# Performance work log

Hardware: AMD Instinct MI355X
Metric: run time of the kernel (lower is better)

## Reference

```python
import jax, jax.numpy as jnp
import numpy as np

B, L, D = 2, 2048, 2048
H, G, HS = 32, 8, 64  # n_heads, n_query_groups, head_size
NEG = -1e30


def setup_inputs() -> dict:
    key = jax.random.key(0)
    ks = jax.random.split(key, 7)
    s = 1.0 / np.sqrt(D)
    return {
        "x": jax.random.normal(ks[0], (B, L, D), jnp.float32),
        "cos": jax.random.uniform(ks[1], (L, HS), jnp.float32),
        "sin": jax.random.uniform(ks[2], (L, HS), jnp.float32),
        "Wq": jax.random.normal(ks[3], (D, D), jnp.float32) * s,
        "Wk": jax.random.normal(ks[4], (G * HS, D), jnp.float32) * s,
        "Wv": jax.random.normal(ks[5], (G * HS, D), jnp.float32) * s,
        "Wo": jax.random.normal(ks[6], (D, D), jnp.float32) * s,
    }


def _apply_rope(t, cos, sin):
    # t: (B, h, L, HS); cos/sin: (L, HS) broadcast over (B, h)
    x1, x2 = t[..., : HS // 2], t[..., HS // 2 :]
    rotated = jnp.concatenate((-x2, x1), axis=-1)
    return (t * cos + rotated * sin).astype(t.dtype)


def reference(x, cos, sin, Wq, Wk, Wv, Wo):
    # projections (torch Linear: y = x @ W.T)
    q = jnp.einsum("bld,ed->ble", x, Wq).reshape(B, L, H, HS).transpose(0, 2, 1, 3)
    k = jnp.einsum("bld,ed->ble", x, Wk).reshape(B, L, G, HS).transpose(0, 2, 1, 3)
    v = jnp.einsum("bld,ed->ble", x, Wv).reshape(B, L, G, HS).transpose(0, 2, 1, 3)
    q = _apply_rope(q, cos, sin)
    k = _apply_rope(k, cos, sin)
    # GQA expand: each group repeated H//G consecutive times (matches expand+reshape)
    k = jnp.repeat(k, H // G, axis=1)
    v = jnp.repeat(v, H // G, axis=1)
    scale = 1.0 / np.sqrt(HS)
    scores = jnp.einsum("bhqd,bhkd->bhqk", q, k) * scale
    causal = jnp.tril(jnp.ones((L, L), bool))
    scores = jnp.where(causal, scores, NEG)
    attn = jax.nn.softmax(scores, axis=-1)
    o = jnp.einsum("bhqk,bhkd->bhqd", attn, v)  # (B,H,L,HS)
    o = o.transpose(0, 2, 1, 3).reshape(B, L, D)
    return jnp.einsum("bld,ed->ble", o, Wo)
```

## Files before the change

### kernel.cpp

```cpp
#include <hip/hip_runtime.h>

typedef __bf16 bf16;
typedef __bf16 bf16x4 __attribute__((ext_vector_type(4)));
typedef __bf16 bf16x8 __attribute__((ext_vector_type(8)));
typedef float  f32x4  __attribute__((ext_vector_type(4)));
typedef float  f32x16 __attribute__((ext_vector_type(16)));

#define GLDS16(gsrc, ldst)                                                    \
  __builtin_amdgcn_global_load_lds(                                          \
      (const __attribute__((address_space(1))) void*)(gsrc),                 \
      (__attribute__((address_space(3))) void*)(ldst), 16, 0, 0)

#define MFMA16(a, b, c) __builtin_amdgcn_mfma_f32_16x16x32_bf16((a), (b), (c), 0, 0, 0)
#define MFMA32(a, b, c) __builtin_amdgcn_mfma_f32_32x32x16_bf16((a), (b), (c), 0, 0, 0)
#define PLSWAP(a, b) asm volatile("v_permlane32_swap_b32 %0, %1" : "+v"(a), "+v"(b))

__device__ inline unsigned pk2(float a, float b) {
  union { bf16 h[2]; unsigned u; } t;
  t.h[0] = (bf16)a; t.h[1] = (bf16)b;
  return t.u;
}
__device__ inline float ex2(float x) { return __builtin_amdgcn_exp2f(x); }

__global__ __launch_bounds__(256) void cvt5_kernel(const float* __restrict__ x,
                                                   const float* __restrict__ wq,
                                                   const float* __restrict__ wk,
                                                   const float* __restrict__ wv,
                                                   const float* __restrict__ wo,
                                                   bf16* __restrict__ xb,
                                                   bf16* __restrict__ wqkv,
                                                   bf16* __restrict__ wob) {
  int i = blockIdx.x * 256 + threadIdx.x;
  const float* src; bf16* dst; int off;
  if (i < 2097152)      { src = x;  dst = xb;             off = i; }
  else if (i < 3145728) { src = wq; dst = wqkv;           off = i - 2097152; }
  else if (i < 3407872) { src = wk; dst = wqkv + 4194304; off = i - 3145728; }
  else if (i < 3670016) { src = wv; dst = wqkv + 5242880; off = i - 3407872; }
  else                  { src = wo; dst = wob;            off = i - 3670016; }
  f32x4 f = *(const f32x4*)(src + (size_t)off * 4);
  bf16x4 o4;
#pragma unroll
  for (int j = 0; j < 4; ++j) o4[j] = (bf16)f[j];
  *(bf16x4*)(dst + (size_t)off * 4) = o4;
}

__global__ __launch_bounds__(256) void vtr_kernel(const bf16* __restrict__ v,
                                                  bf16* __restrict__ vt) {
  constexpr int L = 2048, QS = 3072;
  const int kv0 = blockIdx.x * 64;
  const int bg = blockIdx.y;
  const int tid = threadIdx.x;
  __shared__ bf16 t[64 * 64];

#pragma unroll
  for (int i = 0; i < 2; ++i) {
    int c = tid + 256 * i;
    int kv = c >> 3, e = c & 7;
    bf16x8 row = *(const bf16x8*)(v + (size_t)((bg >> 3) * L + kv0 + kv) * QS +
                                  (bg & 7) * 64 + e * 8);
#pragma unroll
    for (int j = 0; j < 8; ++j)
      t[(8 * e + j) * 64 + (kv ^ (8 * (e ^ j)))] = row[j];
  }
  __syncthreads();

  const int d = tid >> 2, c4 = tid & 3;
  bf16* orow = vt + ((size_t)bg * 64 + d) * L + kv0;
#pragma unroll
  for (int dl = 0; dl < 2; ++dl) {
    int sc = 2 * c4 + dl;
    bf16x8 ch = *(const bf16x8*)&t[d * 64 + 8 * (sc ^ (d >> 3))];
    *(bf16x8*)(orow + 8 * sc) = ch;
  }
}

template <typename OutT, bool ROPE>
__global__ __launch_bounds__(256) void gemm_bt32(const bf16* __restrict__ A,
                                                 const bf16* __restrict__ Bm,
                                                 OutT* __restrict__ C,
                                                 int M, int N, int K,
                                                 const float* __restrict__ cosb,
                                                 const float* __restrict__ sinb) {
  __shared__ bf16 a_lds[128 * 32];
  __shared__ bf16 b_lds[128 * 32];
  const int tid = threadIdx.x;
  const int w = tid >> 6, lane = tid & 63;
  const int lr = lane & 15, lg = lane >> 4;
  const int wr = w >> 1, wc = w & 1;
  const int nbx = N >> 7;
  const int nwg = (M >> 7) * nbx;
  const int bid = blockIdx.x;
  const int sid = (bid & 7) * (nwg >> 3) + (bid >> 3);
  const int m0 = (sid / nbx) << 7, n0 = (sid % nbx) << 7;

  f32x4 acc[4][4];
#pragma unroll
  for (int i = 0; i < 4; ++i)
#pragma unroll
    for (int j = 0; j < 4; ++j) acc[i][j] = f32x4{0.f, 0.f, 0.f, 0.f};

  const int srow = tid >> 2, skc = (tid & 3) * 8;
  const bf16* ap0 = A  + (size_t)(m0 + srow) * K + skc;
  const bf16* ap1 = A  + (size_t)(m0 + srow + 64) * K + skc;
  const bf16* bp0 = Bm + (size_t)(n0 + srow) * K + skc;
  const bf16* bp1 = Bm + (size_t)(n0 + srow + 64) * K + skc;
  bf16* const lA0 = &a_lds[w * 512];
  bf16* const lA1 = &a_lds[w * 512 + 2048];
  bf16* const lB0 = &b_lds[w * 512];
  bf16* const lB1 = &b_lds[w * 512 + 2048];

  for (int kt = 0; kt < K; kt += 32) {
    GLDS16(ap0, lA0);
    GLDS16(ap1, lA1);
    GLDS16(bp0, lB0);
    GLDS16(bp1, lB1);
    ap0 += 32; ap1 += 32; bp0 += 32; bp1 += 32;
    __syncthreads();
    bf16x8 af[4], bfr[4];
#pragma unroll
    for (int t = 0; t < 4; ++t) {
      af[t]  = *(const bf16x8*)&a_lds[(wr * 64 + t * 16 + lr) * 32 + lg * 8];
      bfr[t] = *(const bf16x8*)&b_lds[(wc * 64 + t * 16 + lr) * 32 + lg * 8];
    }
#pragma unroll
    for (int mt = 0; mt < 4; ++mt)
#pragma unroll
      for (int nt = 0; nt < 4; ++nt)
        acc[mt][nt] = MFMA16(af[mt], bfr[nt], acc[mt][nt]);
    __syncthreads();
  }

  const int hb = (n0 + wc * 64) >> 6;
  const bool dorope = ROPE && (hb < 40);
  const float rsc = (ROPE && hb < 32) ? 0.18033688011112042f : 1.0f;

#pragma unroll
  for (int mt = 0; mt < 4; ++mt)
#pragma unroll
    for (int r = 0; r < 4; ++r) {
      int mm = m0 + wr * 64 + mt * 16 + 4 * lg + r;
      float ov[4];
      if (dorope) {
        int l = mm & 2047;
        const float* cp = cosb + l * 64 + lr;
        const float* sp = sinb + l * 64 + lr;
        float a0 = acc[mt][0][r], a1 = acc[mt][1][r];
        float a2 = acc[mt][2][r], a3 = acc[mt][3][r];
        ov[0] = (a0 * cp[0]  - a2 * sp[0])  * rsc;
        ov[1] = (a1 * cp[16] - a3 * sp[16]) * rsc;
        ov[2] = (a2 * cp[32] + a0 * sp[32]) * rsc;
        ov[3] = (a3 * cp[48] + a1 * sp[48]) * rsc;
      } else {
#pragma unroll
        for (int nt = 0; nt < 4; ++nt) ov[nt] = acc[mt][nt][r];
      }
#pragma unroll
      for (int nt = 0; nt < 4; ++nt) {
        int nn = n0 + wc * 64 + nt * 16 + lr;
        C[(size_t)mm * N + nn] = (OutT)ov[nt];
      }
    }
}

template <typename OutT>
__global__ __launch_bounds__(256) void gemm_bt64(const bf16* __restrict__ A,
                                                 const bf16* __restrict__ Bm,
                                                 OutT* __restrict__ C,
                                                 int M, int N, int K) {
  __shared__ bf16 a_lds[128 * 64];
  __shared__ bf16 b_lds[128 * 64];
  const int tid = threadIdx.x;
  const int w = tid >> 6, lane = tid & 63;
  const int lr = lane & 15, lg = lane >> 4;
  const int wr = w >> 1, wc = w & 1;
  const int nbx = N >> 7;
  const int nwg = (M >> 7) * nbx;
  const int bid = blockIdx.x;
  const int sid = (bid & 7) * (nwg >> 3) + (bid >> 3);
  const int m0 = (sid / nbx) << 7, n0 = (sid % nbx) << 7;

  f32x4 acc[4][4];
#pragma unroll
  for (int i = 0; i < 4; ++i)
#pragma unroll
    for (int j = 0; j < 4; ++j) acc[i][j] = f32x4{0.f, 0.f, 0.f, 0.f};

  const bf16* ap[4];
  const bf16* bp[4];
#pragma unroll
  for (int i = 0; i < 4; ++i) {
    int ci = tid + 256 * i;
    int row = ci >> 3, c = ci & 7;
    int cs = c ^ (row & 7);
    ap[i] = A  + (size_t)(m0 + row) * K + cs * 8;
    bp[i] = Bm + (size_t)(n0 + row) * K + cs * 8;
  }

  for (int kt = 0; kt < K; kt += 64) {
#pragma unroll
    for (int i = 0; i < 4; ++i) {
      GLDS16(ap[i], &a_lds[w * 512 + i * 2048]);
      GLDS16(bp[i], &b_lds[w * 512 + i * 2048]);
      ap[i] += 64; bp[i] += 64;
    }
    __syncthreads();
    bf16x8 af[4][2], bfr[4][2];
#pragma unroll
    for (int t = 0; t < 4; ++t) {
      int ra = wr * 64 + t * 16 + lr;
      int rb = wc * 64 + t * 16 + lr;
#pragma unroll
      for (int kc = 0; kc < 2; ++kc) {
        af[t][kc]  = *(const bf16x8*)&a_lds[ra * 64 + (((4 * kc + lg) ^ (ra & 7)) * 8)];
        bfr[t][kc] = *(const bf16x8*)&b_lds[rb * 64 + (((4 * kc + lg) ^ (rb & 7)) * 8)];
      }
    }
#pragma unroll
    for (int mt = 0; mt < 4; ++mt)
#pragma unroll
      for (int nt = 0; nt < 4; ++nt)
#pragma unroll
        for (int kc = 0; kc < 2; ++kc)
          acc[mt][nt] = MFMA16(af[mt][kc], bfr[nt][kc], acc[mt][nt]);
    __syncthreads();
  }

#pragma unroll
  for (int mt = 0; mt < 4; ++mt)
#pragma unroll
    for (int r = 0; r < 4; ++r) {
      int mm = m0 + wr * 64 + mt * 16 + 4 * lg + r;
#pragma unroll
      for (int nt = 0; nt < 4; ++nt) {
        int nn = n0 + wc * 64 + nt * 16 + lr;
        C[(size_t)mm * N + nn] = (OutT)acc[mt][nt][r];
      }
    }
}

__global__ __launch_bounds__(256, 4) void attn_kernel(const bf16* __restrict__ q,
                                                      const bf16* __restrict__ k,
                                                      const bf16* __restrict__ vtg,
                                                      bf16* __restrict__ o,
                                                      bf16* __restrict__ opart,
                                                      float* __restrict__ mpart,
                                                      float* __restrict__ lpart,
                                                      int split_n, int umax) {
  constexpr int L = 2048;
  constexpr int QS = 3072;
  constexpr int OS = 2048;
  const int id = blockIdx.x;
  int bh, u, ts, te, pidx;
  bool split;
  if (id < split_n) {
    bh = id & 63;
    int t = id >> 6;
    u = 15 - (t >> 1);
    int s = t & 1;
    ts = s * (u + 1);
    te = ts + (u + 1);
    pidx = (bh * 9 + (u - 7)) * 2 + s;
    split = true;
  } else {
    int e = id - split_n;
    bh = e & 63;
    u = umax - (e >> 6);
    ts = 0;
    te = 2 * u + 2;
    pidx = 0;
    split = false;
  }
  const int q0 = u * 128;
  const int b = bh >> 5, h = bh & 31, g = h >> 2;
  const int tid = threadIdx.x;
  const int w = tid >> 6, lane = tid & 63;
  const int lc = lane & 31;
  const int H  = lane >> 5;
  const int off4 = 4 * H;
  const int qw = q0 + w * 32;
  const int qg = qw + lc;

  __shared__ bf16 k_lds[2][64 * 64];
  __shared__ bf16 vt_lds[2][64 * 64];

  bf16x8 qf[4];
  {
    const bf16* qrow = q + (size_t)(b * L + qg) * QS + h * 64 + 8 * H;
#pragma unroll
    for (int s = 0; s < 4; ++s) qf[s] = *(const bf16x8*)(qrow + 16 * s);
  }

  f32x16 acc0, acc1;
#pragma unroll
  for (int r = 0; r < 16; ++r) { acc0[r] = 0.f; acc1[r] = 0.f; }
  float m_run = -1e30f, l_run = 0.f;

  const bf16* vbase = vtg + (size_t)(b * 8 + g) * 64 * L;

  const int kvr = tid >> 3, c8 = tid & 7;
  const bf16* kp0 = k + (size_t)(b * L + ts * 64 + kvr) * QS + g * 64 + ((c8 ^ (kvr & 7)) * 8);
  const bf16* kp1 = kp0 + (size_t)32 * QS;
  const bf16* vp0 = vbase + (size_t)kvr * L + ts * 64 + c8 * 8;
  const bf16* vp1 = vp0 + (size_t)32 * L;

  auto stageK = [&](int buf) {
    GLDS16(kp0, &k_lds[buf][w * 512]);
    GLDS16(kp1, &k_lds[buf][w * 512 + 2048]);
    kp0 += (size_t)64 * QS; kp1 += (size_t)64 * QS;
  };
  auto stageV = [&](int buf) {
    GLDS16(vp0, &vt_lds[buf][w * 512]);
    GLDS16(vp1, &vt_lds[buf][w * 512 + 2048]);
    vp0 += 64; vp1 += 64;
  };

  stageK(0);
  stageV(0);
  __syncthreads();

  for (int it = ts; it < te; ++it) {
    const int cur = (it - ts) & 1;
    const int kv0 = it * 64;
    const bool notlast = (it + 1 < te);
    if (notlast) {
      stageK(cur ^ 1);
      stageV(cur ^ 1);
    }

    if (kv0 <= qw + 31) {
      f32x16 p0, p1;
#pragma unroll
      for (int r = 0; r < 16; ++r) { p0[r] = 0.f; p1[r] = 0.f; }
      __builtin_amdgcn_s_setprio(1);
#pragma unroll
      for (int s = 0; s < 4; ++s) {
        int ch = ((2 * s + H) ^ (lc & 7)) * 8;
        bf16x8 kf0 = *(const bf16x8*)&k_lds[cur][lc * 64 + ch];
        bf16x8 kf1 = *(const bf16x8*)&k_lds[cur][(32 + lc) * 64 + ch];
        p0 = MFMA32(kf0, qf[s], p0);
        p1 = MFMA32(kf1, qf[s], p1);
      }
      __builtin_amdgcn_s_setprio(0);

      if (kv0 + 63 > qw) {
#pragma unroll
        for (int r = 0; r < 16; ++r) {
          int kvl = kv0 + (r & 3) + 8 * (r >> 2) + off4;
          if (kvl > qg)      p0[r] = -1e30f;
          if (kvl + 32 > qg) p1[r] = -1e30f;
        }
      }

      float mt = -1e30f;
#pragma unroll
      for (int r = 0; r < 16; ++r) mt = fmaxf(mt, fmaxf(p0[r], p1[r]));
      mt = fmaxf(mt, __shfl_xor(mt, 32));
      const int defer = __all(mt <= m_run + 11.0f);
      float alpha = 1.f;
      if (!defer) {
        float mn = fmaxf(m_run, mt);
        alpha = ex2(m_run - mn);
        m_run = mn;
      }
      float ls = 0.f;
#pragma unroll
      for (int r = 0; r < 16; ++r) {
        p0[r] = ex2(p0[r] - m_run);
        p1[r] = ex2(p1[r] - m_run);
        ls += p0[r] + p1[r];
      }
      ls += __shfl_xor(ls, 32);
      l_run = l_run * alpha + ls;
      if (!defer) {
#pragma unroll
        for (int r = 0; r < 16; ++r) {
          float aq = __shfl(alpha, ((r & 3) + 8 * (r >> 2)) + off4);
          acc0[r] *= aq;
          acc1[r] *= aq;
        }
      }

      unsigned A[16];
#pragma unroll
      for (int i = 0; i < 8; ++i) {
        A[i]     = pk2(p0[2 * i], p0[2 * i + 1]);
        A[8 + i] = pk2(p1[2 * i], p1[2 * i + 1]);
      }
#pragma unroll
      for (int base = 0; base < 16; base += 4) {
        PLSWAP(A[base],     A[base + 2]);
        PLSWAP(A[base + 1], A[base + 3]);
      }

      __builtin_amdgcn_s_setprio(1);
#pragma unroll
      for (int sp = 0; sp < 4; ++sp) {
        union { unsigned u[4]; bf16x8 v8; } pa;
#pragma unroll
        for (int jx = 0; jx < 4; ++jx) pa.u[jx] = A[4 * sp + jx];
        int ch = ((2 * sp + H) ^ (lc & 7)) * 8;
        bf16x8 vf0 = *(const bf16x8*)&vt_lds[cur][lc * 64 + ch];
        bf16x8 vf1 = *(const bf16x8*)&vt_lds[cur][(32 + lc) * 64 + ch];
        acc0 = MFMA32(pa.v8, vf0, acc0);
        acc1 = MFMA32(pa.v8, vf1, acc1);
      }
      __builtin_amdgcn_s_setprio(0);
    }

    __syncthreads();
  }

  if (split) {
    bf16* op = opart + (size_t)pidx * (128 * 64);
#pragma unroll
    for (int r = 0; r < 16; ++r) {
      int qrow = w * 32 + (r & 3) + 8 * (r >> 2) + off4;
      op[qrow * 64 + lc]      = (bf16)acc0[r];
      op[qrow * 64 + 32 + lc] = (bf16)acc1[r];
    }
    if (H == 0) {
      mpart[(size_t)pidx * 128 + w * 32 + lc] = m_run;
      lpart[(size_t)pidx * 128 + w * 32 + lc] = l_run;
    }
  } else {
#pragma unroll
    for (int r = 0; r < 16; ++r) {
      int qrow = (r & 3) + 8 * (r >> 2) + off4;
      float lq = __shfl(l_run, qrow);
      float inv = 1.f / lq;
      size_t orow = (size_t)(b * L + qw + qrow) * OS + h * 64;
      o[orow + lc]      = (bf16)(acc0[r] * inv);
      o[orow + 32 + lc] = (bf16)(acc1[r] * inv);
    }
  }
}

__global__ __launch_bounds__(256) void comb_kernel(const bf16* __restrict__ opart,
                                                   const float* __restrict__ mpart,
                                                   const float* __restrict__ lpart,
                                                   bf16* __restrict__ o) {
  constexpr int L = 2048, OS = 2048;
  const int blk = blockIdx.x;
  const int bh = blk / 9, uu = blk % 9, u = uu + 7;
  const int b = bh >> 5, h = bh & 31;
  const int q0 = u * 128;
  const int t = threadIdx.x;
  const int row = t >> 1, dh = (t & 1) * 32;

  const size_t s0 = (size_t)blk * 2, s1 = s0 + 1;
  float m0 = mpart[s0 * 128 + row], m1 = mpart[s1 * 128 + row];
  float l0 = lpart[s0 * 128 + row], l1 = lpart[s1 * 128 + row];
  float m = fmaxf(m0, m1);
  float w0 = ex2(m0 - m), w1 = ex2(m1 - m);
  float inv = 1.f / (l0 * w0 + l1 * w1);

  const bf16* O0 = opart + s0 * (128 * 64) + row * 64 + dh;
  const bf16* O1 = opart + s1 * (128 * 64) + row * 64 + dh;
  bf16* orow = o + (size_t)(b * L + q0 + row) * OS + h * 64 + dh;
#pragma unroll
  for (int j = 0; j < 4; ++j) {
    bf16x8 a = *(const bf16x8*)(O0 + 8 * j);
    bf16x8 c = *(const bf16x8*)(O1 + 8 * j);
    bf16x8 r;
#pragma unroll
    for (int e = 0; e < 8; ++e)
      r[e] = (bf16)(((float)a[e] * w0 + (float)c[e] * w1) * inv);
    *(bf16x8*)(orow + 8 * j) = r;
  }
}

extern "C" void kernel_launch(void* const* d_in, const int* in_sizes, int n_in,
                              void* d_out, int out_size, void* d_ws, size_t ws_size,
                              hipStream_t stream) {
  (void)in_sizes; (void)n_in; (void)out_size;
  const float* x    = (const float*)d_in[0];
  const float* cosb = (const float*)d_in[1];
  const float* sinb = (const float*)d_in[2];
  const float* Wq   = (const float*)d_in[3];
  const float* Wk   = (const float*)d_in[4];
  const float* Wv   = (const float*)d_in[5];
  const float* Wo   = (const float*)d_in[6];

  constexpr int B = 2, L = 2048, D = 2048, H = 32, G = 8;
  constexpr int M = B * L;
  constexpr int DKV = G * 64;
  constexpr int NQKV = D + 2 * DKV;

  char* p = (char*)d_ws;
  bf16*  xb   = (bf16*)p;  p += (size_t)M * D * 2;
  bf16*  wqkv = (bf16*)p;  p += (size_t)NQKV * D * 2;
  bf16*  wob  = (bf16*)p;  p += (size_t)D * D * 2;
  bf16*  qkv  = (bf16*)p;  p += (size_t)M * NQKV * 2;
  bf16*  vtg  = (bf16*)p;  p += (size_t)B * G * 64 * L * 2;
  bf16*  opart = (bf16*)p; p += (size_t)1152 * 128 * 64 * 2;
  float* mpart = (float*)p; p += (size_t)1152 * 128 * 4;
  float* lpart = (float*)p; p += (size_t)1152 * 128 * 4;
  bf16*  ob   = xb;

  const bool do_split = ws_size >= (size_t)(p - (char*)d_ws);

  cvt5_kernel<<<dim3(18432), 256, 0, stream>>>(x, Wq, Wk, Wv, Wo, xb, wqkv, wob);

  gemm_bt32<bf16, true><<<dim3((NQKV / 128) * (M / 128)), 256, 0, stream>>>(
      xb, wqkv, qkv, M, NQKV, D, cosb, sinb);

  vtr_kernel<<<dim3(L / 64, B * G), 256, 0, stream>>>(qkv + D + DKV, vtg);

  if (do_split) {
    attn_kernel<<<dim3(1600), 256, 0, stream>>>(qkv, qkv + D, vtg, ob,
                                                opart, mpart, lpart, 1152, 6);
    comb_kernel<<<dim3(576), 256, 0, stream>>>(opart, mpart, lpart, ob);
  } else {
    attn_kernel<<<dim3(1024), 256, 0, stream>>>(qkv, qkv + D, vtg, ob,
                                                opart, mpart, lpart, 0, 15);
  }

  gemm_bt64<float><<<dim3((D / 128) * (M / 128)), 256, 0, stream>>>(
      ob, wob, (float*)d_out, M, D, D);
}
```

Before: 213.6 us.

## Split long causal attention rows into 2-4 KV chunks for better balance

Adds a finer split-KV schedule: query tiles u>=12 split into 4 KV chunks, 8-11 into 3, 4-7 into 2, with short tiles unsplit, giving 2560 attention blocks. The combine kernel is generalized to merge a variable number of partials per row. This aims to reduce tail imbalance from the causal triangle, at the cost of more partial-output traffic and workspace, falling back to the old schedule if workspace is too small.

```diff
diff --git a/kernel.cpp b/kernel.cpp
--- a/kernel.cpp
+++ b/kernel.cpp
@@ -245,30 +245,52 @@
                                                       bf16* __restrict__ opart,
                                                       float* __restrict__ mpart,
                                                       float* __restrict__ lpart,
-                                                      int split_n, int umax) {
+                                                      int mode) {
   constexpr int L = 2048;
   constexpr int QS = 3072;
   constexpr int OS = 2048;
   const int id = blockIdx.x;
-  int bh, u, ts, te, pidx;
+  int bh, u, t0, t1, pidx;
   bool split;
-  if (id < split_n) {
+  if (mode == 2) {
+    if (id < 2304) {
+      bh = id & 63;
+      int j = id >> 6, s, ns;
+      if (j < 16)      { u = 15 - (j >> 2); s = j & 3; ns = 4; }
+      else if (j < 28) { int jj = j - 16; u = 11 - jj / 3; s = jj % 3; ns = 3; }
+      else             { int jj = j - 28; u = 7 - (jj >> 1); s = jj & 1; ns = 2; }
+      int T = 2 * u + 2;
+      t0 = s * T / ns;
+      t1 = (s + 1) * T / ns;
+      int basep = (u >= 12) ? 4 * u - 28 : (u >= 8) ? 3 * u - 16 : 2 * u - 8;
+      pidx = bh * 36 + basep + s;
+      split = true;
+    } else {
+      int e = id - 2304;
+      bh = e & 63;
+      u = 3 - (e >> 6);
+      t0 = 0; t1 = 2 * u + 2; pidx = 0; split = false;
+    }
+  } else if (mode == 1) {
+    if (id < 1152) {
+      bh = id & 63;
+      int t = id >> 6;
+      u = 15 - (t >> 1);
+      int s = t & 1;
+      t0 = s * (u + 1);
+      t1 = t0 + (u + 1);
+      pidx = (bh * 9 + (u - 7)) * 2 + s;
+      split = true;
+    } else {
+      int e = id - 1152;
+      bh = e & 63;
+      u = 6 - (e >> 6);
+      t0 = 0; t1 = 2 * u + 2; pidx = 0; split = false;
+    }
+  } else {
     bh = id & 63;
-    int t = id >> 6;
-    u = 15 - (t >> 1);
-    int s = t & 1;
-    ts = s * (u + 1);
-    te = ts + (u + 1);
-    pidx = (bh * 9 + (u - 7)) * 2 + s;
-    split = true;
-  } else {
-    int e = id - split_n;
-    bh = e & 63;
-    u = umax - (e >> 6);
-    ts = 0;
-    te = 2 * u + 2;
-    pidx = 0;
-    split = false;
+    u = 15 - (id >> 6);
+    t0 = 0; t1 = 2 * u + 2; pidx = 0; split = false;
   }
   const int q0 = u * 128;
   const int b = bh >> 5, h = bh & 31, g = h >> 2;
@@ -298,9 +320,9 @@
   const bf16* vbase = vtg + (size_t)(b * 8 + g) * 64 * L;
 
   const int kvr = tid >> 3, c8 = tid & 7;
-  const bf16* kp0 = k + (size_t)(b * L + ts * 64 + kvr) * QS + g * 64 + ((c8 ^ (kvr & 7)) * 8);
+  const bf16* kp0 = k + (size_t)(b * L + t0 * 64 + kvr) * QS + g * 64 + ((c8 ^ (kvr & 7)) * 8);
   const bf16* kp1 = kp0 + (size_t)32 * QS;
-  const bf16* vp0 = vbase + (size_t)kvr * L + ts * 64 + c8 * 8;
+  const bf16* vp0 = vbase + (size_t)kvr * L + t0 * 64 + c8 * 8;
   const bf16* vp1 = vp0 + (size_t)32 * L;
 
   auto stageK = [&](int buf) {
@@ -318,10 +340,10 @@
   stageV(0);
   __syncthreads();
 
-  for (int it = ts; it < te; ++it) {
-    const int cur = (it - ts) & 1;
+  for (int it = t0; it < t1; ++it) {
+    const int cur = (it - t0) & 1;
     const int kv0 = it * 64;
-    const bool notlast = (it + 1 < te);
+    const bool notlast = (it + 1 < t1);
     if (notlast) {
       stageK(cur ^ 1);
       stageV(cur ^ 1);
@@ -438,33 +460,52 @@
 __global__ __launch_bounds__(256) void comb_kernel(const bf16* __restrict__ opart,
                                                    const float* __restrict__ mpart,
                                                    const float* __restrict__ lpart,
-                                                   bf16* __restrict__ o) {
+                                                   bf16* __restrict__ o, int mode) {
   constexpr int L = 2048, OS = 2048;
   const int blk = blockIdx.x;
-  const int bh = blk / 9, uu = blk % 9, u = uu + 7;
+  int u, bh, ns;
+  size_t slot0;
+  if (mode == 2) {
+    u = 4 + blk % 12;
+    bh = blk / 12;
+    ns = (u >= 12) ? 4 : (u >= 8) ? 3 : 2;
+    int basep = (u >= 12) ? 4 * u - 28 : (u >= 8) ? 3 * u - 16 : 2 * u - 8;
+    slot0 = (size_t)bh * 36 + basep;
+  } else {
+    u = 7 + blk % 9;
+    bh = blk / 9;
+    ns = 2;
+    slot0 = ((size_t)bh * 9 + (u - 7)) * 2;
+  }
   const int b = bh >> 5, h = bh & 31;
   const int q0 = u * 128;
   const int t = threadIdx.x;
   const int row = t >> 1, dh = (t & 1) * 32;
 
-  const size_t s0 = (size_t)blk * 2, s1 = s0 + 1;
-  float m0 = mpart[s0 * 128 + row], m1 = mpart[s1 * 128 + row];
-  float l0 = lpart[s0 * 128 + row], l1 = lpart[s1 * 128 + row];
-  float m = fmaxf(m0, m1);
-  float w0 = ex2(m0 - m), w1 = ex2(m1 - m);
-  float inv = 1.f / (l0 * w0 + l1 * w1);
-
-  const bf16* O0 = opart + s0 * (128 * 64) + row * 64 + dh;
-  const bf16* O1 = opart + s1 * (128 * 64) + row * 64 + dh;
+  float m = -1e30f;
+  for (int s = 0; s < ns; ++s) m = fmaxf(m, mpart[(slot0 + s) * 128 + row]);
+  float wgt[4];
+  float l = 0.f;
+  for (int s = 0; s < ns; ++s) {
+    wgt[s] = ex2(mpart[(slot0 + s) * 128 + row] - m);
+    l += lpart[(slot0 + s) * 128 + row] * wgt[s];
+  }
+  float inv = 1.f / l;
+
   bf16* orow = o + (size_t)(b * L + q0 + row) * OS + h * 64 + dh;
 #pragma unroll
   for (int j = 0; j < 4; ++j) {
-    bf16x8 a = *(const bf16x8*)(O0 + 8 * j);
-    bf16x8 c = *(const bf16x8*)(O1 + 8 * j);
+    float a8[8];
+#pragma unroll
+    for (int e = 0; e < 8; ++e) a8[e] = 0.f;
+    for (int s = 0; s < ns; ++s) {
+      bf16x8 a = *(const bf16x8*)(opart + (slot0 + s) * 8192 + row * 64 + dh + 8 * j);
+#pragma unroll
+      for (int e = 0; e < 8; ++e) a8[e] += (float)a[e] * wgt[s];
+    }
     bf16x8 r;
 #pragma unroll
-    for (int e = 0; e < 8; ++e)
-      r[e] = (bf16)(((float)a[e] * w0 + (float)c[e] * w1) * inv);
+    for (int e = 0; e < 8; ++e) r[e] = (bf16)(a8[e] * inv);
     *(bf16x8*)(orow + 8 * j) = r;
   }
 }
@@ -492,12 +533,19 @@
   bf16*  wob  = (bf16*)p;  p += (size_t)D * D * 2;
   bf16*  qkv  = (bf16*)p;  p += (size_t)M * NQKV * 2;
   bf16*  vtg  = (bf16*)p;  p += (size_t)B * G * 64 * L * 2;
-  bf16*  opart = (bf16*)p; p += (size_t)1152 * 128 * 64 * 2;
-  float* mpart = (float*)p; p += (size_t)1152 * 128 * 4;
-  float* lpart = (float*)p; p += (size_t)1152 * 128 * 4;
   bf16*  ob   = xb;
 
-  const bool do_split = ws_size >= (size_t)(p - (char*)d_ws);
+  const size_t base_off = (size_t)(p - (char*)d_ws);
+  const size_t slot_o = 128 * 64 * 2;
+  auto need = [&](size_t S) { return base_off + S * (slot_o + 2 * 128 * 4); };
+  int mode; size_t S;
+  if (ws_size >= need(2304))      { mode = 2; S = 2304; }
+  else if (ws_size >= need(1152)) { mode = 1; S = 1152; }
+  else                            { mode = 0; S = 0; }
+
+  bf16*  opart = (bf16*)p;  p += S * slot_o;
+  float* mpart = (float*)p; p += S * 128 * 4;
+  float* lpart = (float*)p; p += S * 128 * 4;
 
   cvt5_kernel<<<dim3(18432), 256, 0, stream>>>(x, Wq, Wk, Wv, Wo, xb, wqkv, wob);
 
@@ -506,13 +554,17 @@
 
   vtr_kernel<<<dim3(L / 64, B * G), 256, 0, stream>>>(qkv + D + DKV, vtg);
 
-  if (do_split) {
+  if (mode == 2) {
+    attn_kernel<<<dim3(2560), 256, 0, stream>>>(qkv, qkv + D, vtg, ob,
+                                                opart, mpart, lpart, 2);
+    comb_kernel<<<dim3(768), 256, 0, stream>>>(opart, mpart, lpart, ob, 2);
+  } else if (mode == 1) {
     attn_kernel<<<dim3(1600), 256, 0, stream>>>(qkv, qkv + D, vtg, ob,
-                                                opart, mpart, lpart, 1152, 6);
-    comb_kernel<<<dim3(576), 256, 0, stream>>>(opart, mpart, lpart, ob);
+                                                opart, mpart, lpart, 1);
+    comb_kernel<<<dim3(576), 256, 0, stream>>>(opart, mpart, lpart, ob, 1);
   } else {
     attn_kernel<<<dim3(1024), 256, 0, stream>>>(qkv, qkv + D, vtg, ob,
-                                                opart, mpart, lpart, 0, 15);
+                                                opart, mpart, lpart, 0);
   }
 
   gemm_bt64<float><<<dim3((D / 128) * (M / 128)), 256, 0, stream>>>(
```

Result: slower. 228.2 us (+6.8%).
